# Optimization experiments

Measured on AMD Instinct MI355X. Metric: run time of the kernel, lower is better.

## Reference

```python
import jax, jax.numpy as jnp
import numpy as np

B, N, D = 256, 133, 1024
H, C = 8, 128  # per-head channels; H*C == out_channels
NEG_SLOPE = 0.2


def setup_inputs() -> dict:
    key = jax.random.key(0)
    kx, kw, ka, kadj = jax.random.split(key, 4)
    x = jax.random.normal(kx, (B, N, D), dtype=jnp.float32)
    W = jax.random.normal(kw, (H * C, D), dtype=jnp.float32) * 0.02  # nn.Linear weight (out,in)
    attn_w = jax.random.normal(ka, (2 * C,), dtype=jnp.float32) * 0.02  # attn Linear(2C,1) weight
    # binary adjacency with self-loops so every softmax column has a valid entry
    bern = (jax.random.uniform(kadj, (N, N)) < 0.15).astype(jnp.float32)
    adj = jnp.maximum(bern, jnp.eye(N, dtype=jnp.float32))[:, :, None]  # (N,N,1)
    return {"x": x, "W": W, "attn_w": attn_w, "adj": adj}


def reference(x, W, attn_w, adj):
    b, n, _ = x.shape
    g = (x @ W.T).reshape(b, n, H, C)  # (B,N,H,C)
    # concat(g_j, g_i) @ attn_w == g_j @ wl + g_i @ wr (leakyrelu applied after the sum)
    wl, wr = attn_w[:C], attn_w[C:]
    sj = jnp.einsum('bnhc,c->bnh', g, wl)  # score contribution from g[b, j]
    si = jnp.einsum('bnhc,c->bnh', g, wr)  # score contribution from g[b, i]
    e = jax.nn.leaky_relu(si[:, :, None, :] + sj[:, None, :, :], NEG_SLOPE)  # (B,N,N,H) e[b,i,j,h]
    e = jnp.where(adj[None] == 0, -jnp.inf, e)
    a = jax.nn.softmax(e, axis=1)  # faithful to original: softmax over dim=1 (the i axis)
    # dropout omitted (inference/eval mode)
    out = jnp.einsum('bijh,bjhf->bihf', a, g)  # aggregate over j
    return out.reshape(b, n, H * C)  # is_concat=True
```

## Files before the change

kernel.cpp:

```cpp
#include <hip/hip_runtime.h>

#define NB    133
#define NBP   136
#define BATCH 256
#define HEADS 8
#define CDIM  128
#define DDIM  1024
#define MROWS (BATCH * NB)
#define NDIM  (HEADS * CDIM)
#define BH    (BATCH * HEADS)
#define NKT   32

typedef __bf16 bf16_t;
typedef bf16_t bf16x8 __attribute__((ext_vector_type(8)));
typedef float  f32x4  __attribute__((ext_vector_type(4)));

__device__ __forceinline__ unsigned short f2bf(float f) {
  unsigned u = __float_as_uint(f);
  u += 0x7fffu + ((u >> 16) & 1u);
  return (unsigned short)(u >> 16);
}
__device__ __forceinline__ void load_lds16(const void* g, void* l) {
  __builtin_amdgcn_global_load_lds(
      (__attribute__((address_space(1))) void*)(g),
      (__attribute__((address_space(3))) void*)(l), 16, 0, 0);
}
__device__ __forceinline__ void bar() {
  asm volatile("" ::: "memory");
  __builtin_amdgcn_s_barrier();
  asm volatile("" ::: "memory");
}
#define VMWAIT(n) asm volatile("s_waitcnt vmcnt(" #n ")" ::: "memory")

__global__ __launch_bounds__(256) void cvt_kernel(const float* __restrict__ x,
                                                  const float* __restrict__ W,
                                                  unsigned short* __restrict__ xb,
                                                  unsigned short* __restrict__ wb) {
  const int nx = MROWS * DDIM / 8, nw = NDIM * DDIM / 8;
  int i = blockIdx.x * 256 + threadIdx.x;
  const float* src; unsigned short* dst; int k;
  if (i < nx)           { src = x; dst = xb; k = i; }
  else if (i < nx + nw) { src = W; dst = wb; k = i - nx; }
  else return;
  const float4* s4 = (const float4*)src;
  float4 a = s4[(size_t)k * 2];
  float4 b = s4[(size_t)k * 2 + 1];
  union { unsigned short u[8]; uint4 v; } p;
  p.u[0] = f2bf(a.x); p.u[1] = f2bf(a.y); p.u[2] = f2bf(a.z); p.u[3] = f2bf(a.w);
  p.u[4] = f2bf(b.x); p.u[5] = f2bf(b.y); p.u[6] = f2bf(b.z); p.u[7] = f2bf(b.w);
  ((uint4*)dst)[k] = p.v;
}

__global__ __launch_bounds__(192) void mask_kernel(const float* __restrict__ adj,
                                                   unsigned* __restrict__ rm,
                                                   unsigned* __restrict__ cm) {
  const int tid = threadIdx.x, lane = tid & 63, wv = tid >> 6, blk = blockIdx.x;
  if (blk < 144) {
    const int i = blk;
    bool on = (i < NB) && (tid < NB) && (adj[i * NB + tid] != 0.f);
    unsigned long long bb = __ballot(on);
    if (lane == 0)  rm[i * 6 + wv * 2]     = (unsigned)bb;
    if (lane == 32) rm[i * 6 + wv * 2 + 1] = (unsigned)(bb >> 32);
  } else {
    const int j = blk - 144;
    bool on = (tid < NB) && (adj[tid * NB + j] != 0.f);
    unsigned long long bb = __ballot(on);
    if (lane == 0)  cm[j * 6 + wv * 2]     = (unsigned)bb;
    if (lane == 32) cm[j * 6 + wv * 2 + 1] = (unsigned)(bb >> 32);
  }
}

__global__ __launch_bounds__(256, 2) void gemm_kernel(const unsigned short* __restrict__ xb,
                                                      const unsigned short* __restrict__ wb,
                                                      const float* __restrict__ attn_w,
                                                      unsigned short* __restrict__ gb,
                                                      float* __restrict__ si_ws,
                                                      float* __restrict__ sj_ws) {
  __shared__ __attribute__((aligned(16))) unsigned short Abuf[3][128 * 32];
  __shared__ __attribute__((aligned(16))) unsigned short Bbuf[3][256 * 32];
  __shared__ float sred[2][4][128];

  const int tid = threadIdx.x;
  const int orig = blockIdx.x;
  const int wg = (orig & 7) * 133 + (orig >> 3);
  const int bn = wg & 3, bm = wg >> 2;

  const int lane = tid & 63, w = tid >> 6;
  const int q = lane >> 4, li = lane & 15;

  const unsigned short* Ab = xb + (size_t)bm * 128 * DDIM;
  const unsigned short* Bb = wb + (size_t)bn * 256 * DDIM;

  int sA[2], sB[4];
#pragma unroll
  for (int i = 0; i < 2; ++i) {
    const int f = tid + i * 256;
    sA[i] = (f >> 2) * DDIM + (((f & 3) ^ ((f >> 2) & 3)) << 3);
  }
#pragma unroll
  for (int i = 0; i < 4; ++i) {
    const int f = tid + i * 256;
    sB[i] = (f >> 2) * DDIM + (((f & 3) ^ ((f >> 2) & 3)) << 3);
  }
#define STGA(buf_, kt_) do { \
    load_lds16(Ab + sA[0] + (kt_) * 32, &Abuf[buf_][tid * 8]); \
    load_lds16(Ab + sA[1] + (kt_) * 32, &Abuf[buf_][(tid + 256) * 8]); \
  } while (0)
#define STGB(buf_, kt_) do { \
    load_lds16(Bb + sB[0] + (kt_) * 32, &Bbuf[buf_][tid * 8]); \
    load_lds16(Bb + sB[1] + (kt_) * 32, &Bbuf[buf_][(tid + 256) * 8]); \
    load_lds16(Bb + sB[2] + (kt_) * 32, &Bbuf[buf_][(tid + 512) * 8]); \
    load_lds16(Bb + sB[3] + (kt_) * 32, &Bbuf[buf_][(tid + 768) * 8]); \
  } while (0)

  const int asl = (q ^ (li & 3)) << 3;

  f32x4 acc[8][4] = {};
  bf16x8 a[8], bf01[2], bf23[2];

  STGA(0, 0); STGB(0, 0);
  STGA(1, 1); STGB(1, 1);
  VMWAIT(6);
  bar();

  for (int t = 0; t < NKT; ++t) {
    const int cur = t % 3, nxt = (t + 2) % 3;
    const unsigned short* As = &Abuf[cur][0];
    const unsigned short* Bs = &Bbuf[cur][0];
#pragma unroll
    for (int mi = 0; mi < 8; ++mi)
      a[mi] = *(const bf16x8*)&As[(mi * 16 + li) * 32 + asl];
#pragma unroll
    for (int ni = 0; ni < 2; ++ni)
      bf01[ni] = *(const bf16x8*)&Bs[(w * 64 + ni * 16 + li) * 32 + asl];
    bar();
    __builtin_amdgcn_s_setprio(1);
#pragma unroll
    for (int mi = 0; mi < 8; ++mi)
#pragma unroll
      for (int ni = 0; ni < 2; ++ni)
        acc[mi][ni] = __builtin_amdgcn_mfma_f32_16x16x32_bf16(a[mi], bf01[ni], acc[mi][ni], 0, 0, 0);
    __builtin_amdgcn_s_setprio(0);
#pragma unroll
    for (int ni = 0; ni < 2; ++ni)
      bf23[ni] = *(const bf16x8*)&Bs[(w * 64 + (ni + 2) * 16 + li) * 32 + asl];
    if (t < NKT - 2) {
      STGA(nxt, t + 2); STGB(nxt, t + 2);
      VMWAIT(6);
    } else {
      VMWAIT(0);
    }
    bar();
    __builtin_amdgcn_s_setprio(1);
#pragma unroll
    for (int mi = 0; mi < 8; ++mi)
#pragma unroll
      for (int ni = 0; ni < 2; ++ni)
        acc[mi][ni + 2] = __builtin_amdgcn_mfma_f32_16x16x32_bf16(a[mi], bf23[ni], acc[mi][ni + 2], 0, 0, 0);
    __builtin_amdgcn_s_setprio(0);
  }
#undef STGA
#undef STGB

  float wlv[4], wrv[4];
#pragma unroll
  for (int ni = 0; ni < 4; ++ni) {
    const int cc = (w & 1) * 64 + ni * 16 + li;
    wlv[ni] = attn_w[cc];
    wrv[ni] = attn_w[CDIM + cc];
  }
#pragma unroll
  for (int mi = 0; mi < 8; ++mi)
#pragma unroll
    for (int rr = 0; rr < 4; ++rr) {
      float pj = 0.f, pi = 0.f;
#pragma unroll
      for (int ni = 0; ni < 4; ++ni) {
        pj += acc[mi][ni][rr] * wlv[ni];
        pi += acc[mi][ni][rr] * wrv[ni];
      }
#pragma unroll
      for (int d = 1; d < 16; d <<= 1) {
        pj += __shfl_xor(pj, d);
        pi += __shfl_xor(pi, d);
      }
      if (li == 0) {
        sred[0][w][mi * 16 + q * 4 + rr] = pj;
        sred[1][w][mi * 16 + q * 4 + rr] = pi;
      }
    }
  __syncthreads();
#pragma unroll
  for (int idx0 = 0; idx0 < 2; ++idx0) {
    const int idx = idx0 * 256 + tid;
    const int row = idx & 127;
    const int hw = (idx >> 7) & 1;
    const int which = idx >> 8;
    const float v = sred[which][hw * 2][row] + sred[which][hw * 2 + 1][row];
    const int rg = bm * 128 + row;
    const int b = rg / NB, n = rg - b * NB;
    const int h = bn * 2 + hw;
    float* dst = which ? si_ws : sj_ws;
    dst[(b * HEADS + h) * NB + n] = v;
  }

#pragma unroll
  for (int mi = 0; mi < 8; ++mi)
#pragma unroll
    for (int ni = 0; ni < 4; ++ni) {
      const int col = bn * 256 + w * 64 + ni * 16 + li;
      const size_t row0 = (size_t)(bm * 128 + mi * 16 + q * 4);
#pragma unroll
      for (int rr = 0; rr < 4; ++rr)
        gb[(row0 + rr) * NDIM + col] = f2bf(acc[mi][ni][rr]);
    }
}

__global__ __launch_bounds__(192) void stats_kernel(const float* __restrict__ si_ws,
                                                    const float* __restrict__ sj_ws,
                                                    const unsigned* __restrict__ cm,
                                                    float2* __restrict__ smrg) {
  __shared__ float siL[NB];
  const int tid = threadIdx.x;
  const int base = blockIdx.x * NB;
  if (tid < NB) siL[tid] = si_ws[base + tid];
  __syncthreads();
  if (tid >= 160) return;
  float2 o = {0.f, 0.f};
  if (tid < NB) {
    const int j = tid;
    const float sjv = sj_ws[base + j];
    float m = -3.0e38f;
#pragma unroll
    for (int wd = 0; wd < 5; ++wd) {
      unsigned bits = cm[j * 6 + wd];
      while (bits) {
        const int i = __ffs(bits) - 1; bits &= bits - 1;
        float e = siL[wd * 32 + i] + sjv;
        e = e > 0.f ? e : 0.2f * e;
        m = fmaxf(m, e);
      }
    }
    float s = 0.f;
#pragma unroll
    for (int wd = 0; wd < 5; ++wd) {
      unsigned bits = cm[j * 6 + wd];
      while (bits) {
        const int i = __ffs(bits) - 1; bits &= bits - 1;
        float e = siL[wd * 32 + i] + sjv;
        e = e > 0.f ? e : 0.2f * e;
        s += __expf(e - m);
      }
    }
    o.x = sjv;
    o.y = m + __logf(s);
  }
  smrg[(size_t)blockIdx.x * 160 + tid] = o;
}

__global__ __launch_bounds__(256) void agg_kernel(const unsigned short* __restrict__ gb,
                                                  const float* __restrict__ si_ws,
                                                  const float2* __restrict__ smrg,
                                                  const unsigned* __restrict__ rm,
                                                  float* __restrict__ out) {
  __shared__ __attribute__((aligned(16))) unsigned short gTl[64 * NBP + 32];
  __shared__ __attribute__((aligned(8))) float2 smrL[160];
  const int tid = threadIdx.x;
  const int bh = blockIdx.x >> 1, fh = blockIdx.x & 1;
  const int b = bh >> 3, h = bh & 7;
  const int base = bh * NB;

  if (tid < 64) {
    gTl[tid * NBP + 133] = 0;
    *(unsigned*)&gTl[tid * NBP + 134] = 0;
  }
  if (tid >= 64 && tid < 80) *(unsigned*)&gTl[64 * NBP + 2 * (tid - 64)] = 0;
  if (tid < 160) smrL[tid] = smrg[(size_t)bh * 160 + tid];

  const unsigned short* gsrc = gb + (size_t)(b * NB) * NDIM + h * CDIM + fh * 64;
  for (int u = tid; u < NB * 16; u += 256) {
    const int j = u >> 4, fg = u & 15;
    const uint2 d = *(const uint2*)(gsrc + (size_t)j * NDIM + fg * 4);
    const int f0 = fg * 4;
    gTl[(f0 + 0) * NBP + j] = (unsigned short)(d.x);
    gTl[(f0 + 1) * NBP + j] = (unsigned short)(d.x >> 16);
    gTl[(f0 + 2) * NBP + j] = (unsigned short)(d.y);
    gTl[(f0 + 3) * NBP + j] = (unsigned short)(d.y >> 16);
  }
  __syncthreads();

  const int lane = tid & 63, wv = tid >> 6, q = lane >> 4, li = lane & 15;
  for (int mt = wv; mt < 9; mt += 4) {
    const int il = mt * 16 + li;
    const float si_r = si_ws[base + (il < NB ? il : NB - 1)];
    const unsigned* rmr = rm + il * 6;
    f32x4 acc[4] = {};
#pragma unroll
    for (int ks = 0; ks < 5; ++ks) {
      const int j0 = ks * 32 + q * 8;
      const unsigned bits = rmr[ks] >> (q * 8);
      bf16x8 afv;
#pragma unroll
      for (int jj = 0; jj < 8; ++jj) {
        const float2 sv = smrL[j0 + jj];
        float e = si_r + sv.x;
        e = e > 0.f ? e : 0.2f * e;
        const float wgt = ((bits >> jj) & 1u) ? __expf(e - sv.y) : 0.f;
        afv[jj] = (bf16_t)wgt;
      }
#pragma unroll
      for (int n = 0; n < 4; ++n) {
        const bf16x8 bv = *(const bf16x8*)&gTl[(n * 16 + li) * NBP + j0];
        acc[n] = __builtin_amdgcn_mfma_f32_16x16x32_bf16(afv, bv, acc[n], 0, 0, 0);
      }
    }
    float* obase = out + (size_t)(b * NB) * NDIM + h * CDIM + fh * 64;
#pragma unroll
    for (int n = 0; n < 4; ++n)
#pragma unroll
      for (int rr = 0; rr < 4; ++rr) {
        const int i = mt * 16 + q * 4 + rr;
        if (i < NB) obase[(size_t)i * NDIM + n * 16 + li] = acc[n][rr];
      }
  }
}

extern "C" void kernel_launch(void* const* d_in, const int* in_sizes, int n_in,
                              void* d_out, int out_size, void* d_ws, size_t ws_size,
                              hipStream_t stream) {
  const float* x      = (const float*)d_in[0];
  const float* W      = (const float*)d_in[1];
  const float* attn_w = (const float*)d_in[2];
  const float* adj    = (const float*)d_in[3];
  float* out = (float*)d_out;
  char* ws = (char*)d_ws;

  unsigned short* xb = (unsigned short*)(ws + 0);
  unsigned short* wb = (unsigned short*)(ws + 69730304);
  unsigned short* gb = (unsigned short*)(ws + 71827456);
  float* si = (float*)(ws + 141557760);
  float* sj = (float*)(ws + 142647296);
  unsigned* rm = (unsigned*)(ws + 143736832);
  unsigned* cm = (unsigned*)(ws + 143740288);
  float2* smrg = (float2*)(ws + 0);

  const int ncvt = (MROWS * DDIM + NDIM * DDIM) / 8;
  cvt_kernel<<<(ncvt + 255) / 256, 256, 0, stream>>>(x, W, xb, wb);
  mask_kernel<<<277, 192, 0, stream>>>(adj, rm, cm);
  gemm_kernel<<<266 * 4, 256, 0, stream>>>(xb, wb, attn_w, gb, si, sj);
  stats_kernel<<<BH, 192, 0, stream>>>(si, sj, cm, smrg);
  agg_kernel<<<BH * 2, 256, 0, stream>>>(gb, si, smrg, rm, out);
}
```

Measured before the change: 437.3 us.

## Load GEMM B operand straight to registers and drop its LDS staging

```diff
diff --git a/kernel.cpp b/kernel.cpp
--- a/kernel.cpp
+++ b/kernel.cpp
@@ -77,7 +77,6 @@
                                                       float* __restrict__ si_ws,
                                                       float* __restrict__ sj_ws) {
   __shared__ __attribute__((aligned(16))) unsigned short Abuf[3][128 * 32];
-  __shared__ __attribute__((aligned(16))) unsigned short Bbuf[3][256 * 32];
   __shared__ float sred[2][4][128];
 
   const int tid = threadIdx.x;
@@ -89,78 +88,65 @@
   const int q = lane >> 4, li = lane & 15;
 
   const unsigned short* Ab = xb + (size_t)bm * 128 * DDIM;
-  const unsigned short* Bb = wb + (size_t)bn * 256 * DDIM;
-
-  int sA[2], sB[4];
-#pragma unroll
-  for (int i = 0; i < 2; ++i) {
-    const int f = tid + i * 256;
-    sA[i] = (f >> 2) * DDIM + (((f & 3) ^ ((f >> 2) & 3)) << 3);
-  }
-#pragma unroll
-  for (int i = 0; i < 4; ++i) {
-    const int f = tid + i * 256;
-    sB[i] = (f >> 2) * DDIM + (((f & 3) ^ ((f >> 2) & 3)) << 3);
-  }
-#define STGA(buf_, kt_) do { \
-    load_lds16(Ab + sA[0] + (kt_) * 32, &Abuf[buf_][tid * 8]); \
-    load_lds16(Ab + sA[1] + (kt_) * 32, &Abuf[buf_][(tid + 256) * 8]); \
+
+  int sA0, sA1;
+  { int f = tid;       sA0 = (f >> 2) * DDIM + ((((f & 3) ^ ((f >> 4) & 3))) << 3); }
+  { int f = tid + 256; sA1 = (f >> 2) * DDIM + ((((f & 3) ^ ((f >> 4) & 3))) << 3); }
+#define STGA(dst_, kt_) do { \
+    load_lds16(Ab + sA0 + (kt_) * 32, (dst_) + tid * 8); \
+    load_lds16(Ab + sA1 + (kt_) * 32, (dst_) + (tid + 256) * 8); \
   } while (0)
-#define STGB(buf_, kt_) do { \
-    load_lds16(Bb + sB[0] + (kt_) * 32, &Bbuf[buf_][tid * 8]); \
-    load_lds16(Bb + sB[1] + (kt_) * 32, &Bbuf[buf_][(tid + 256) * 8]); \
-    load_lds16(Bb + sB[2] + (kt_) * 32, &Bbuf[buf_][(tid + 512) * 8]); \
-    load_lds16(Bb + sB[3] + (kt_) * 32, &Bbuf[buf_][(tid + 768) * 8]); \
-  } while (0)
-
-  const int asl = (q ^ (li & 3)) << 3;
+
+  const unsigned short* Bp = wb + (size_t)(bn * 256 + w * 64 + li) * DDIM + q * 8;
+
+  const int asl = (q ^ (li >> 2)) << 3;
 
   f32x4 acc[8][4] = {};
-  bf16x8 a[8], bf01[2], bf23[2];
-
-  STGA(0, 0); STGB(0, 0);
-  STGA(1, 1); STGB(1, 1);
+  bf16x8 a[8], bE[4], bO[4];
+
+  unsigned short* p0 = &Abuf[0][0];
+  unsigned short* p1 = &Abuf[1][0];
+  unsigned short* p2 = &Abuf[2][0];
+
+#define LDA_(src_) { _Pragma("unroll") for (int mi = 0; mi < 8; ++mi) \
+      a[mi] = *(const bf16x8*)&(src_)[(mi * 16 + li) * 32 + asl]; }
+#define LDB(dst_, kt_) { _Pragma("unroll") for (int ni = 0; ni < 4; ++ni) \
+      dst_[ni] = *(const bf16x8*)(Bp + ni * 16 * DDIM + (kt_) * 32); }
+#define MM(bv_) { __builtin_amdgcn_s_setprio(1); \
+      _Pragma("unroll") for (int ni = 0; ni < 4; ++ni) \
+      _Pragma("unroll") for (int mi = 0; mi < 8; ++mi) \
+        acc[mi][ni] = __builtin_amdgcn_mfma_f32_16x16x32_bf16(a[mi], bv_[ni], acc[mi][ni], 0, 0, 0); \
+      __builtin_amdgcn_s_setprio(0); }
+
+  STGA(p0, 0); STGA(p1, 1);
+  LDB(bE, 0);
   VMWAIT(6);
   bar();
 
-  for (int t = 0; t < NKT; ++t) {
-    const int cur = t % 3, nxt = (t + 2) % 3;
-    const unsigned short* As = &Abuf[cur][0];
-    const unsigned short* Bs = &Bbuf[cur][0];
-#pragma unroll
-    for (int mi = 0; mi < 8; ++mi)
-      a[mi] = *(const bf16x8*)&As[(mi * 16 + li) * 32 + asl];
-#pragma unroll
-    for (int ni = 0; ni < 2; ++ni)
-      bf01[ni] = *(const bf16x8*)&Bs[(w * 64 + ni * 16 + li) * 32 + asl];
+  for (int t = 0; t < 28; t += 2) {
+    LDA_(p0);
+    STGA(p2, t + 2);
+    LDB(bO, t + 1);
+    VMWAIT(6);
     bar();
-    __builtin_amdgcn_s_setprio(1);
-#pragma unroll
-    for (int mi = 0; mi < 8; ++mi)
-#pragma unroll
-      for (int ni = 0; ni < 2; ++ni)
-        acc[mi][ni] = __builtin_amdgcn_mfma_f32_16x16x32_bf16(a[mi], bf01[ni], acc[mi][ni], 0, 0, 0);
-    __builtin_amdgcn_s_setprio(0);
-#pragma unroll
-    for (int ni = 0; ni < 2; ++ni)
-      bf23[ni] = *(const bf16x8*)&Bs[(w * 64 + (ni + 2) * 16 + li) * 32 + asl];
-    if (t < NKT - 2) {
-      STGA(nxt, t + 2); STGB(nxt, t + 2);
-      VMWAIT(6);
-    } else {
-      VMWAIT(0);
-    }
+    MM(bE);
+    LDA_(p1);
+    STGA(p0, t + 3);
+    LDB(bE, t + 2);
+    VMWAIT(6);
     bar();
-    __builtin_amdgcn_s_setprio(1);
-#pragma unroll
-    for (int mi = 0; mi < 8; ++mi)
-#pragma unroll
-      for (int ni = 0; ni < 2; ++ni)
-        acc[mi][ni + 2] = __builtin_amdgcn_mfma_f32_16x16x32_bf16(a[mi], bf23[ni], acc[mi][ni + 2], 0, 0, 0);
-    __builtin_amdgcn_s_setprio(0);
-  }
+    MM(bO);
+    unsigned short* tmp = p0; p0 = p2; p2 = p1; p1 = tmp;
+  }
+  LDA_(p0); STGA(p2, 30); LDB(bO, 29); VMWAIT(6); bar(); MM(bE);
+  LDA_(p1); STGA(p0, 31); LDB(bE, 30); VMWAIT(6); bar(); MM(bO);
+  { unsigned short* tmp = p0; p0 = p2; p2 = p1; p1 = tmp; }
+  LDA_(p0); LDB(bO, 31); VMWAIT(6); bar(); MM(bE);
+  LDA_(p1); MM(bO);
 #undef STGA
-#undef STGB
+#undef LDA_
+#undef LDB
+#undef MM
 
   float wlv[4], wrv[4];
 #pragma unroll
```

Result: slower. 453.6 us (+3.7%).

## Precompute attention weights once per head in LDS and retune GEMM swizzle

Applied to the files above, without the earlier changes.

```diff
diff --git a/kernel.cpp b/kernel.cpp
--- a/kernel.cpp
+++ b/kernel.cpp
@@ -2,6 +2,7 @@
 
 #define NB    133
 #define NBP   136
+#define NJP   168
 #define BATCH 256
 #define HEADS 8
 #define CDIM  128
@@ -95,12 +96,12 @@
 #pragma unroll
   for (int i = 0; i < 2; ++i) {
     const int f = tid + i * 256;
-    sA[i] = (f >> 2) * DDIM + (((f & 3) ^ ((f >> 2) & 3)) << 3);
+    sA[i] = (f >> 2) * DDIM + (((f & 3) ^ ((f >> 3) & 3)) << 3);
   }
 #pragma unroll
   for (int i = 0; i < 4; ++i) {
     const int f = tid + i * 256;
-    sB[i] = (f >> 2) * DDIM + (((f & 3) ^ ((f >> 2) & 3)) << 3);
+    sB[i] = (f >> 2) * DDIM + (((f & 3) ^ ((f >> 3) & 3)) << 3);
   }
 #define STGA(buf_, kt_) do { \
     load_lds16(Ab + sA[0] + (kt_) * 32, &Abuf[buf_][tid * 8]); \
@@ -113,7 +114,7 @@
     load_lds16(Bb + sB[3] + (kt_) * 32, &Bbuf[buf_][(tid + 768) * 8]); \
   } while (0)
 
-  const int asl = (q ^ (li & 3)) << 3;
+  const int asl = (q ^ ((li >> 1) & 3)) << 3;
 
   f32x4 acc[8][4] = {};
   bf16x8 a[8], bf01[2], bf23[2];
@@ -258,70 +259,86 @@
   smrg[(size_t)blockIdx.x * 160 + tid] = o;
 }
 
-__global__ __launch_bounds__(256) void agg_kernel(const unsigned short* __restrict__ gb,
+__global__ __launch_bounds__(512) void agg_kernel(const unsigned short* __restrict__ gb,
                                                   const float* __restrict__ si_ws,
                                                   const float2* __restrict__ smrg,
                                                   const unsigned* __restrict__ rm,
                                                   float* __restrict__ out) {
-  __shared__ __attribute__((aligned(16))) unsigned short gTl[64 * NBP + 32];
-  __shared__ __attribute__((aligned(8))) float2 smrL[160];
+  __shared__ __attribute__((aligned(16))) unsigned short wLs[144 * NJP];
+  __shared__ __attribute__((aligned(16))) unsigned short gTl[128 * NJP];
   const int tid = threadIdx.x;
-  const int bh = blockIdx.x >> 1, fh = blockIdx.x & 1;
+  const int bh = blockIdx.x;
   const int b = bh >> 3, h = bh & 7;
   const int base = bh * NB;
-
-  if (tid < 64) {
-    gTl[tid * NBP + 133] = 0;
-    *(unsigned*)&gTl[tid * NBP + 134] = 0;
-  }
-  if (tid >= 64 && tid < 80) *(unsigned*)&gTl[64 * NBP + 2 * (tid - 64)] = 0;
-  if (tid < 160) smrL[tid] = smrg[(size_t)bh * 160 + tid];
-
-  const unsigned short* gsrc = gb + (size_t)(b * NB) * NDIM + h * CDIM + fh * 64;
-  for (int u = tid; u < NB * 16; u += 256) {
-    const int j = u >> 4, fg = u & 15;
+  const float2* smr = smrg + (size_t)bh * 160;
+
+  for (int e = tid; e < 133 * 17; e += 512) {
+    const int i = e / 17, t = e - i * 17;
+    *(unsigned*)&wLs[i * NJP + 134 + 2 * t] = 0;
+  }
+  for (int e = tid; e < 11 * 84; e += 512) {
+    const int r = 133 + e / 84, t = e - (e / 84) * 84;
+    *(unsigned*)&wLs[r * NJP + 2 * t] = 0;
+  }
+  for (int e = tid; e < 128 * 18; e += 512) {
+    const int f = e / 18, k = e - f * 18;
+    if (k == 0) wLs[0] += 0, gTl[f * NJP + 133] = 0;
+    else *(unsigned*)&gTl[f * NJP + 132 + 2 * k] = 0;
+  }
+
+  for (int e = tid; e < 133 * 67; e += 512) {
+    const int i = e / 67, jp = e - i * 67;
+    const int j0 = jp * 2;
+    const float si_r = si_ws[base + i];
+    const unsigned bits = rm[i * 6 + (j0 >> 5)];
+    float v0, v1;
+    {
+      const float2 sv = smr[j0];
+      float ee = si_r + sv.x;
+      ee = ee > 0.f ? ee : 0.2f * ee;
+      v0 = ((bits >> (j0 & 31)) & 1u) ? __expf(ee - sv.y) : 0.f;
+    }
+    if (j0 + 1 < 133) {
+      const float2 sv = smr[j0 + 1];
+      float ee = si_r + sv.x;
+      ee = ee > 0.f ? ee : 0.2f * ee;
+      v1 = ((bits >> ((j0 + 1) & 31)) & 1u) ? __expf(ee - sv.y) : 0.f;
+    } else v1 = 0.f;
+    *(unsigned*)&wLs[i * NJP + j0] = (unsigned)f2bf(v0) | ((unsigned)f2bf(v1) << 16);
+  }
+
+  const unsigned short* gsrc = gb + (size_t)(b * NB) * NDIM + h * CDIM;
+  for (int u = tid; u < NB * 32; u += 512) {
+    const int j = u >> 5, fg = u & 31;
     const uint2 d = *(const uint2*)(gsrc + (size_t)j * NDIM + fg * 4);
     const int f0 = fg * 4;
-    gTl[(f0 + 0) * NBP + j] = (unsigned short)(d.x);
-    gTl[(f0 + 1) * NBP + j] = (unsigned short)(d.x >> 16);
-    gTl[(f0 + 2) * NBP + j] = (unsigned short)(d.y);
-    gTl[(f0 + 3) * NBP + j] = (unsigned short)(d.y >> 16);
+    gTl[(f0 + 0) * NJP + j] = (unsigned short)(d.x);
+    gTl[(f0 + 1) * NJP + j] = (unsigned short)(d.x >> 16);
+    gTl[(f0 + 2) * NJP + j] = (unsigned short)(d.y);
+    gTl[(f0 + 3) * NJP + j] = (unsigned short)(d.y >> 16);
   }
   __syncthreads();
 
   const int lane = tid & 63, wv = tid >> 6, q = lane >> 4, li = lane & 15;
-  for (int mt = wv; mt < 9; mt += 4) {
-    const int il = mt * 16 + li;
-    const float si_r = si_ws[base + (il < NB ? il : NB - 1)];
-    const unsigned* rmr = rm + il * 6;
-    f32x4 acc[4] = {};
+  const int f0 = wv * 16;
+  bf16x8 bv[5];
+#pragma unroll
+  for (int ks = 0; ks < 5; ++ks)
+    bv[ks] = *(const bf16x8*)&gTl[(f0 + li) * NJP + ks * 32 + q * 8];
+  float* obase = out + (size_t)(b * NB) * NDIM + h * CDIM + f0;
+#pragma unroll
+  for (int mt = 0; mt < 9; ++mt) {
+    f32x4 acc = {};
 #pragma unroll
     for (int ks = 0; ks < 5; ++ks) {
-      const int j0 = ks * 32 + q * 8;
-      const unsigned bits = rmr[ks] >> (q * 8);
-      bf16x8 afv;
-#pragma unroll
-      for (int jj = 0; jj < 8; ++jj) {
-        const float2 sv = smrL[j0 + jj];
-        float e = si_r + sv.x;
-        e = e > 0.f ? e : 0.2f * e;
-        const float wgt = ((bits >> jj) & 1u) ? __expf(e - sv.y) : 0.f;
-        afv[jj] = (bf16_t)wgt;
-      }
-#pragma unroll
-      for (int n = 0; n < 4; ++n) {
-        const bf16x8 bv = *(const bf16x8*)&gTl[(n * 16 + li) * NBP + j0];
-        acc[n] = __builtin_amdgcn_mfma_f32_16x16x32_bf16(afv, bv, acc[n], 0, 0, 0);
-      }
-    }
-    float* obase = out + (size_t)(b * NB) * NDIM + h * CDIM + fh * 64;
-#pragma unroll
-    for (int n = 0; n < 4; ++n)
-#pragma unroll
-      for (int rr = 0; rr < 4; ++rr) {
-        const int i = mt * 16 + q * 4 + rr;
-        if (i < NB) obase[(size_t)i * NDIM + n * 16 + li] = acc[n][rr];
-      }
+      const bf16x8 av = *(const bf16x8*)&wLs[(mt * 16 + li) * NJP + ks * 32 + q * 8];
+      acc = __builtin_amdgcn_mfma_f32_16x16x32_bf16(av, bv[ks], acc, 0, 0, 0);
+    }
+#pragma unroll
+    for (int rr = 0; rr < 4; ++rr) {
+      const int i = mt * 16 + q * 4 + rr;
+      if (i < NB) obase[(size_t)i * NDIM + li] = acc[rr];
+    }
   }
 }
 
@@ -349,5 +366,5 @@
   mask_kernel<<<277, 192, 0, stream>>>(adj, rm, cm);
   gemm_kernel<<<266 * 4, 256, 0, stream>>>(xb, wb, attn_w, gb, si, sj);
   stats_kernel<<<BH, 192, 0, stream>>>(si, sj, cm, smrg);
-  agg_kernel<<<BH * 2, 256, 0, stream>>>(gb, si, smrg, rm, out);
-}
+  agg_kernel<<<BH, 512, 0, stream>>>(gb, si, smrg, rm, out);
+}
```

Measured after the change: 472.1 us. +8.0%, slower.
